# Optimization experiments

Measured on AMD Instinct MI355X. Metric: run time of the kernel, lower is better.

Reference implementation:

```python
import jax, jax.numpy as jnp
import numpy as np

B, S, H, NH = 2, 2048, 1024, 16
HD = H // NH  # head_dim = 64


def setup_inputs() -> dict:
    key = jax.random.key(0)
    k1, k2, k3 = jax.random.split(key, 3)
    x = jax.random.normal(k1, (B, S, H), dtype=jnp.float32)
    # additive causal mask: 0 on/below diagonal, -1e9 above
    causal = jnp.tril(jnp.ones((S, S), dtype=bool))
    mask = jnp.where(causal, 0.0, -1e9).astype(jnp.float32)[None, None, :, :]
    # fan-in scaled init like flax Dense default (lecun_normal)
    W_qkv = jax.random.normal(k2, (H, 3 * H), dtype=jnp.float32) / np.sqrt(H)
    W_out = jax.random.normal(k3, (H, H), dtype=jnp.float32) / np.sqrt(H)
    return {"x": x, "mask": mask, "W_qkv": W_qkv, "W_out": W_out}


def reference(x, mask, W_qkv, W_out):
    b, s, _ = x.shape
    qkv = jnp.einsum('bsh,hf->bsf', x, W_qkv)  # [B,S,3H]
    q, k, v = jnp.split(qkv, 3, axis=-1)
    q = q.reshape(b, s, NH, HD)
    k = k.reshape(b, s, NH, HD)
    v = v.reshape(b, s, NH, HD)
    scores = jnp.einsum('bqhd,bkhd->bhqk', q, k) / jnp.sqrt(jnp.float32(HD))
    scores = scores + mask
    attn = jax.nn.softmax(scores, axis=-1)
    y = jnp.einsum('bhqk,bkhd->bqhd', attn, v).reshape(b, s, H)
    return jnp.einsum('bsh,ho->bso', y, W_out)
```

## Files before the change

kernel.cpp:

```cpp
#include <hip/hip_runtime.h>

#define B_ 2
#define S_ 2048
#define H_ 1024
#define NH_ 16
#define HD_ 64

typedef short s16x8 __attribute__((ext_vector_type(8)));
typedef float f32x4 __attribute__((ext_vector_type(4)));

__device__ __forceinline__ ushort f2bf(float f) {
  union { float f; unsigned u; } v;
  v.f = f;
  unsigned r = (v.u + 0x7fffu + ((v.u >> 16) & 1u)) >> 16;
  return (ushort)r;
}

__device__ __forceinline__ void gload16(const void* g, void* l) {
  typedef const __attribute__((address_space(1))) unsigned int* gp_t;
  typedef __attribute__((address_space(3))) unsigned int* lp_t;
  __builtin_amdgcn_global_load_lds((gp_t)g, (lp_t)l, 16, 0, 0);
}

__global__ __launch_bounds__(256) void k_prep(const float* __restrict__ x,
                                              ushort* __restrict__ xb,
                                              const float* __restrict__ Wqkv,
                                              ushort* __restrict__ wqkvT,
                                              const float* __restrict__ Wout,
                                              ushort* __restrict__ woutT) {
  __shared__ ushort tile[32][33];
  const int bid = blockIdx.x;
  if (bid < 4096) {
    int i = bid * 256 + threadIdx.x;
    float4 v = ((const float4*)x)[i];
    ushort4 o;
    o.x = f2bf(v.x); o.y = f2bf(v.y); o.z = f2bf(v.z); o.w = f2bf(v.w);
    ((ushort4*)xb)[i] = o;
    return;
  }
  const float* in;
  ushort* out;
  int R = 1024, C, t;
  if (bid < 7168) { in = Wqkv; out = wqkvT; C = 3072; t = bid - 4096; }
  else            { in = Wout; out = woutT; C = 1024; t = bid - 7168; }
  int nbx = C >> 5;
  int c0 = (t % nbx) * 32, r0 = (t / nbx) * 32;
  int tr = threadIdx.x >> 5, tc = threadIdx.x & 31;
#pragma unroll
  for (int i = 0; i < 4; ++i)
    tile[tr + 8 * i][tc] = f2bf(in[(size_t)(r0 + tr + 8 * i) * C + c0 + tc]);
  __syncthreads();
#pragma unroll
  for (int i = 0; i < 4; ++i)
    out[(size_t)(c0 + tr + 8 * i) * R + r0 + tc] = tile[tc][tr + 8 * i];
}

template <int MODE>
__global__ __launch_bounds__(256) void k_gemm(const ushort* __restrict__ A,
                                              const ushort* __restrict__ Bt,
                                              void* __restrict__ out0,
                                              ushort* __restrict__ outK,
                                              ushort* __restrict__ outV,
                                              int Kdim, int Ndim) {
  __shared__ __align__(16) ushort As[2][128 * 64];
  __shared__ __align__(16) ushort Bs[2][128 * 64];
  const int nwg = gridDim.x * gridDim.y;
  const int id = blockIdx.y * gridDim.x + blockIdx.x;
  const int sid = (id & 7) * (nwg >> 3) + (id >> 3);
  const int m0 = (sid / gridDim.x) * 128, n0 = (sid % gridDim.x) * 128;
  const int tid = threadIdx.x, lane = tid & 63, w = tid >> 6;
  const int g = lane >> 4, c = lane & 15;
  const int wr = w >> 1, wc = w & 1;
  f32x4 acc[4][4] = {};
  const int trow = tid >> 3, tcol = tid & 7;
  const ushort* ag = A + (size_t)(m0 + trow) * Kdim + tcol * 8;
  const ushort* bg = Bt + (size_t)(n0 + trow) * Kdim + tcol * 8;

#define STAGE_G(bf, k0)                                      \
  do {                                                       \
    _Pragma("unroll") for (int i_ = 0; i_ < 4; ++i_) {       \
      gload16(ag + (k0) + i_ * 32 * Kdim, As[bf] + tid * 8 + i_ * 2048); \
      gload16(bg + (k0) + i_ * 32 * Kdim, Bs[bf] + tid * 8 + i_ * 2048); \
    }                                                        \
  } while (0)

  const int nk = Kdim >> 6;
  STAGE_G(0, 0);
  asm volatile("s_waitcnt vmcnt(0)" ::: "memory");
  __builtin_amdgcn_s_barrier();
  __builtin_amdgcn_sched_barrier(0);

  int buf = 0;
#pragma unroll 1
  for (int t = 0; t < nk; ++t) {
    if (t + 1 < nk) STAGE_G(buf ^ 1, (t + 1) * 64);
#pragma unroll
    for (int kk = 0; kk < 64; kk += 32) {
      s16x8 af[4], bfr[4];
#pragma unroll
      for (int i = 0; i < 4; ++i)
        af[i] = *(const s16x8*)(As[buf] + (wr * 64 + i * 16 + c) * 64 + kk + g * 8);
#pragma unroll
      for (int i = 0; i < 4; ++i)
        bfr[i] = *(const s16x8*)(Bs[buf] + (wc * 64 + i * 16 + c) * 64 + kk + g * 8);
      __builtin_amdgcn_s_setprio(1);
#pragma unroll
      for (int i = 0; i < 4; ++i)
#pragma unroll
        for (int j = 0; j < 4; ++j)
          acc[i][j] = __builtin_amdgcn_mfma_f32_16x16x32_bf16(af[i], bfr[j], acc[i][j], 0, 0, 0);
      __builtin_amdgcn_s_setprio(0);
    }
    asm volatile("s_waitcnt vmcnt(0)" ::: "memory");
    __builtin_amdgcn_s_barrier();
    __builtin_amdgcn_sched_barrier(0);
    buf ^= 1;
  }
#undef STAGE_G

  if (MODE == 1) {
    float* out = (float*)out0;
#pragma unroll
    for (int i = 0; i < 4; ++i) {
      int mb = m0 + wr * 64 + i * 16 + g * 4;
#pragma unroll
      for (int j = 0; j < 4; ++j) {
        int n = n0 + wc * 64 + j * 16 + c;
#pragma unroll
        for (int r = 0; r < 4; ++r)
          out[(size_t)(mb + r) * Ndim + n] = acc[i][j][r];
      }
    }
  } else {
    if (n0 < 1024) {
      const float ALPHA = 0.18033688f;
      ushort* outQ = (ushort*)out0;
#pragma unroll
      for (int i = 0; i < 4; ++i) {
        int mb = m0 + wr * 64 + i * 16 + g * 4;
#pragma unroll
        for (int j = 0; j < 4; ++j) {
          int n = n0 + wc * 64 + j * 16 + c;
#pragma unroll
          for (int r = 0; r < 4; ++r)
            outQ[(size_t)(mb + r) * 1024 + n] = f2bf(acc[i][j][r] * ALPHA);
        }
      }
    } else if (n0 < 2048) {
#pragma unroll
      for (int i = 0; i < 4; ++i) {
        int mb = m0 + wr * 64 + i * 16 + g * 4;
#pragma unroll
        for (int j = 0; j < 4; ++j) {
          int n = n0 - 1024 + wc * 64 + j * 16 + c;
#pragma unroll
          for (int r = 0; r < 4; ++r)
            outK[(size_t)(mb + r) * 1024 + n] = f2bf(acc[i][j][r]);
        }
      }
    } else {
#pragma unroll
      for (int i = 0; i < 4; ++i) {
        int mb = m0 + wr * 64 + i * 16 + g * 4;
        int bidx = mb >> 11;
        int s = mb & 2047;
#pragma unroll
        for (int j = 0; j < 4; ++j) {
          int nv = n0 - 2048 + wc * 64 + j * 16 + c;
          int h = nv >> 6, d = nv & 63;
          ushort4 pk;
          pk.x = f2bf(acc[i][j][0]);
          pk.y = f2bf(acc[i][j][1]);
          pk.z = f2bf(acc[i][j][2]);
          pk.w = f2bf(acc[i][j][3]);
          *(ushort4*)(outV + ((size_t)((bidx * 16 + h) * 64 + d)) * 2048 + s) = pk;
        }
      }
    }
  }
}

__global__ __launch_bounds__(256) void k_attn(const ushort* __restrict__ Qb,
                                              const ushort* __restrict__ Kb,
                                              const ushort* __restrict__ Vt,
                                              ushort* __restrict__ Yb) {
  __shared__ __align__(16) ushort Ks[2][64 * 64];
  __shared__ __align__(16) ushort Vs[2][64 * 64];
  __shared__ __align__(16) unsigned int Pp[4][16 * 32];
  const int fid = blockIdx.x;
  const int wid = (fid & 7) * 64 + (fid >> 3);
  const int bh = wid >> 4;
  const int j = wid & 15;
  const int b = bh >> 4, h = bh & 15;
  const int tid = threadIdx.x, w = tid >> 6, lane = tid & 63;
  const int g = lane >> 4, c = lane & 15;
  char* pb = (char*)(&Pp[w][0]);

  const int trow = tid >> 3, tcol = tid & 7;
  const int csrc = tcol ^ (trow & 7);
  const ushort* kgb = Kb + (size_t)(b * S_ + trow) * H_ + h * HD_ + csrc * 8;
  const ushort* vgb = Vt + (size_t)(bh * HD_ + trow) * S_ + csrc * 8;

#define STAGE(bf, tile)                                          \
  do {                                                           \
    int ks_ = (tile) * 64;                                       \
    gload16(kgb + (size_t)ks_ * H_, Ks[bf] + tid * 8);           \
    gload16(kgb + (size_t)(ks_ + 32) * H_, Ks[bf] + 2048 + tid * 8); \
    gload16(vgb + ks_, Vs[bf] + tid * 8);                        \
    gload16(vgb + ks_ + 32 * S_, Vs[bf] + 2048 + tid * 8);       \
  } while (0)

#pragma unroll 1
  for (int half = 0; half < 2; ++half) {
    const int qc = half ? (31 - j) : j;
    const int q0 = qc * 64;
    const int nt = qc + 1;
    const int qw = q0 + w * 16;

    s16x8 qf[2];
#pragma unroll
    for (int dc = 0; dc < 2; ++dc)
      qf[dc] = *(const s16x8*)(Qb + (size_t)(b * S_ + qw + c) * H_ +
                               h * HD_ + dc * 32 + g * 8);

    f32x4 oacc[4] = {};
    float m = -1e30f, lp = 0.f;

    STAGE(0, 0);
    asm volatile("s_waitcnt vmcnt(0)" ::: "memory");
    __builtin_amdgcn_s_barrier();
    __builtin_amdgcn_sched_barrier(0);

    int buf = 0;
#pragma unroll 1
    for (int it = 0; it < nt; ++it) {
      const int ks = it * 64;
      if (it + 1 < nt) STAGE(buf ^ 1, it + 1);

      f32x4 sacc[4] = {};
      __builtin_amdgcn_s_setprio(1);
#pragma unroll
      for (int dc = 0; dc < 2; ++dc) {
#pragma unroll
        for (int kt = 0; kt < 4; ++kt) {
          int R = kt * 16 + c;
          int cc = dc * 4 + g;
          s16x8 kf = *(const s16x8*)((const char*)Ks[buf] + R * 128 + ((cc ^ (R & 7)) << 4));
          sacc[kt] = __builtin_amdgcn_mfma_f32_16x16x32_bf16(kf, qf[dc], sacc[kt], 0, 0, 0);
        }
      }
      __builtin_amdgcn_s_setprio(0);

      if (it == nt - 1) {
        int q = qw + c;
#pragma unroll
        for (int kt = 0; kt < 4; ++kt)
#pragma unroll
          for (int r = 0; r < 4; ++r)
            if (ks + kt * 16 + g * 4 + r > q) sacc[kt][r] = -1e30f;
      }

      float t0 = fmaxf(fmaxf(sacc[0][0], sacc[0][1]), fmaxf(sacc[0][2], sacc[0][3]));
      float t1 = fmaxf(fmaxf(sacc[1][0], sacc[1][1]), fmaxf(sacc[1][2], sacc[1][3]));
      float t2 = fmaxf(fmaxf(sacc[2][0], sacc[2][1]), fmaxf(sacc[2][2], sacc[2][3]));
      float t3 = fmaxf(fmaxf(sacc[3][0], sacc[3][1]), fmaxf(sacc[3][2], sacc[3][3]));
      float t = fmaxf(fmaxf(t0, t1), fmaxf(t2, t3));
      t = fmaxf(t, __shfl_xor(t, 16));
      t = fmaxf(t, __shfl_xor(t, 32));

      if (__any(t > m + 8.0f)) {
        float mnew = fmaxf(m, t);
        float sc = __builtin_amdgcn_exp2f(m - mnew);
        m = mnew;
        lp *= sc;
        float scq[4];
#pragma unroll
        for (int r = 0; r < 4; ++r) scq[r] = __shfl(sc, g * 4 + r);
#pragma unroll
        for (int dt = 0; dt < 4; ++dt)
#pragma unroll
          for (int r = 0; r < 4; ++r) oacc[dt][r] *= scq[r];
      }

      float p[4][4];
      float rs = 0.f;
#pragma unroll
      for (int kt = 0; kt < 4; ++kt)
#pragma unroll
        for (int r = 0; r < 4; ++r) {
          p[kt][r] = __builtin_amdgcn_exp2f(sacc[kt][r] - m);
          rs += p[kt][r];
        }
      lp += rs;
      unsigned int pw[8];
#pragma unroll
      for (int kt = 0; kt < 4; ++kt) {
        asm("v_cvt_pk_bf16_f32 %0, %1, %2" : "=v"(pw[kt * 2 + 0]) : "v"(p[kt][0]), "v"(p[kt][1]));
        asm("v_cvt_pk_bf16_f32 %0, %1, %2" : "=v"(pw[kt * 2 + 1]) : "v"(p[kt][2]), "v"(p[kt][3]));
      }
#pragma unroll
      for (int kt = 0; kt < 4; ++kt) {
        int qd = kt * 2 + (g >> 1);
        *(uint2*)(pb + c * 128 + ((qd ^ (c & 7)) << 4) + ((g & 1) << 3)) =
            make_uint2(pw[kt * 2], pw[kt * 2 + 1]);
      }
      asm volatile("s_waitcnt lgkmcnt(0)" ::: "memory");
      __builtin_amdgcn_sched_barrier(0);

      __builtin_amdgcn_s_setprio(1);
#pragma unroll
      for (int kc = 0; kc < 2; ++kc) {
        int qd = kc * 4 + g;
        s16x8 pf = *(const s16x8*)(pb + c * 128 + ((qd ^ (c & 7)) << 4));
        int cc = kc * 4 + g;
#pragma unroll
        for (int dt = 0; dt < 4; ++dt) {
          int R = dt * 16 + c;
          s16x8 vf = *(const s16x8*)((const char*)Vs[buf] + R * 128 + ((cc ^ (R & 7)) << 4));
          oacc[dt] = __builtin_amdgcn_mfma_f32_16x16x32_bf16(pf, vf, oacc[dt], 0, 0, 0);
        }
      }
      __builtin_amdgcn_s_setprio(0);

      asm volatile("s_waitcnt vmcnt(0)" ::: "memory");
      __builtin_amdgcn_s_barrier();
      __builtin_amdgcn_sched_barrier(0);
      buf ^= 1;
    }

    float lt = lp;
    lt += __shfl_xor(lt, 16);
    lt += __shfl_xor(lt, 32);
    float rq[4];
#pragma unroll
    for (int r = 0; r < 4; ++r) rq[r] = 1.0f / __shfl(lt, g * 4 + r);
#pragma unroll
    for (int dt = 0; dt < 4; ++dt)
#pragma unroll
      for (int r = 0; r < 4; ++r) {
        int s = qw + g * 4 + r;
        Yb[(size_t)(b * S_ + s) * H_ + h * HD_ + dt * 16 + c] = f2bf(oacc[dt][r] * rq[r]);
      }
  }
#undef STAGE
}

extern "C" void kernel_launch(void* const* d_in, const int* in_sizes, int n_in,
                              void* d_out, int out_size, void* d_ws, size_t ws_size,
                              hipStream_t stream) {
  (void)in_sizes; (void)n_in; (void)out_size; (void)ws_size;
  const float* x = (const float*)d_in[0];
  const float* Wqkv = (const float*)d_in[2];
  const float* Wout = (const float*)d_in[3];
  float* out = (float*)d_out;

  char* ws = (char*)d_ws;
  ushort* xb    = (ushort*)(ws + 0);
  ushort* wqkvT = (ushort*)(ws + 8388608);
  ushort* woutT = (ushort*)(ws + 14680064);
  ushort* Qb    = (ushort*)(ws + 16777216);
  ushort* Kb    = (ushort*)(ws + 25165824);
  ushort* Vtb   = (ushort*)(ws + 33554432);
  ushort* Yb    = (ushort*)(ws + 41943040);

  k_prep<<<dim3(8192), dim3(256), 0, stream>>>(x, xb, Wqkv, wqkvT, Wout, woutT);
  k_gemm<0><<<dim3(24, 32), dim3(256), 0, stream>>>(xb, wqkvT, (void*)Qb, Kb, Vtb, 1024, 3072);
  k_attn<<<dim3(512), dim3(256), 0, stream>>>(Qb, Kb, Vtb, Yb);
  k_gemm<1><<<dim3(8, 32), dim3(256), 0, stream>>>(Yb, woutT, (void*)out, nullptr, nullptr, 1024, 1024);
}
```

Measured before the change: 209.5 us.

## Enlarge GEMM tiles to 256x256 with swizzled LDS and interleaved prefetch

Rewrites both projection GEMMs to use 256x256 output tiles with 512-thread blocks and 8 waves. Shared memory uses an XOR-swizzled layout to avoid bank conflicts. Next-tile global-to-LDS loads are split into four stripes and issued between quadrant compute phases, with finer waitcnt and barrier control. This raises reuse of each loaded tile and overlaps loads with MFMA work. The cost is far fewer blocks: 192 for the QKV GEMM and only 64 for the output GEMM, which may leave many CUs idle.

```diff
diff --git a/kernel.cpp b/kernel.cpp
--- a/kernel.cpp
+++ b/kernel.cpp
@@ -56,76 +56,107 @@
 }
 
 template <int MODE>
-__global__ __launch_bounds__(256) void k_gemm(const ushort* __restrict__ A,
-                                              const ushort* __restrict__ Bt,
-                                              void* __restrict__ out0,
-                                              ushort* __restrict__ outK,
-                                              ushort* __restrict__ outV,
-                                              int Kdim, int Ndim) {
-  __shared__ __align__(16) ushort As[2][128 * 64];
-  __shared__ __align__(16) ushort Bs[2][128 * 64];
+__global__ __launch_bounds__(512, 2) void k_gemm(const ushort* __restrict__ A,
+                                                 const ushort* __restrict__ Bt,
+                                                 void* __restrict__ out0,
+                                                 ushort* __restrict__ outK,
+                                                 ushort* __restrict__ outV,
+                                                 int Kdim, int Ndim) {
+  __shared__ __align__(16) ushort As[2][256 * 64];
+  __shared__ __align__(16) ushort Bs[2][256 * 64];
   const int nwg = gridDim.x * gridDim.y;
   const int id = blockIdx.y * gridDim.x + blockIdx.x;
   const int sid = (id & 7) * (nwg >> 3) + (id >> 3);
-  const int m0 = (sid / gridDim.x) * 128, n0 = (sid % gridDim.x) * 128;
+  const int m0 = (sid / gridDim.x) * 256, n0 = (sid % gridDim.x) * 256;
   const int tid = threadIdx.x, lane = tid & 63, w = tid >> 6;
   const int g = lane >> 4, c = lane & 15;
-  const int wr = w >> 1, wc = w & 1;
-  f32x4 acc[4][4] = {};
-  const int trow = tid >> 3, tcol = tid & 7;
-  const ushort* ag = A + (size_t)(m0 + trow) * Kdim + tcol * 8;
-  const ushort* bg = Bt + (size_t)(n0 + trow) * Kdim + tcol * 8;
-
-#define STAGE_G(bf, k0)                                      \
-  do {                                                       \
-    _Pragma("unroll") for (int i_ = 0; i_ < 4; ++i_) {       \
-      gload16(ag + (k0) + i_ * 32 * Kdim, As[bf] + tid * 8 + i_ * 2048); \
-      gload16(bg + (k0) + i_ * 32 * Kdim, Bs[bf] + tid * 8 + i_ * 2048); \
-    }                                                        \
-  } while (0)
-
-  const int nk = Kdim >> 6;
-  STAGE_G(0, 0);
-  asm volatile("s_waitcnt vmcnt(0)" ::: "memory");
+  const int wm = w >> 2, wn = w & 3;
+  f32x4 acc[8][4] = {};
+
+  const int srow = tid >> 3;
+  const int csrc = (tid & 7) ^ (srow & 7);
+  const ushort* ag = A + (size_t)(m0 + srow) * Kdim + csrc * 8;
+  const ushort* bg = Bt + (size_t)(n0 + srow) * Kdim + csrc * 8;
+  const int nT = Kdim >> 6;
+
+#define STRIPE(gp, ro, T_, dst) \
+  gload16((gp) + (size_t)(ro) * Kdim + (T_) * 64, (dst) + tid * 8)
+
+  STRIPE(ag, 0, 0, As[0]); STRIPE(ag, 64, 0, As[0] + 4096);
+  STRIPE(bg, 0, 0, Bs[0]); STRIPE(bg, 64, 0, Bs[0] + 4096);
+  STRIPE(bg, 128, 0, Bs[0] + 8192); STRIPE(bg, 192, 0, Bs[0] + 12288);
+  STRIPE(ag, 128, 0, As[0] + 8192); STRIPE(ag, 192, 0, As[0] + 12288);
+  asm volatile("s_waitcnt vmcnt(4)" ::: "memory");
   __builtin_amdgcn_s_barrier();
   __builtin_amdgcn_sched_barrier(0);
 
-  int buf = 0;
 #pragma unroll 1
-  for (int t = 0; t < nk; ++t) {
-    if (t + 1 < nk) STAGE_G(buf ^ 1, (t + 1) * 64);
-#pragma unroll
-    for (int kk = 0; kk < 64; kk += 32) {
-      s16x8 af[4], bfr[4];
-#pragma unroll
-      for (int i = 0; i < 4; ++i)
-        af[i] = *(const s16x8*)(As[buf] + (wr * 64 + i * 16 + c) * 64 + kk + g * 8);
-#pragma unroll
-      for (int i = 0; i < 4; ++i)
-        bfr[i] = *(const s16x8*)(Bs[buf] + (wc * 64 + i * 16 + c) * 64 + kk + g * 8);
+  for (int t = 0; t < nT; ++t) {
+    const char* Ab = (const char*)As[t & 1];
+    const char* Bb = (const char*)Bs[t & 1];
+    const bool stg = (t + 1 < nT);
+    const int T2 = t + 1, bf2 = T2 & 1;
+#pragma unroll
+    for (int q = 0; q < 4; ++q) {
+      const int ih = q >> 1, jh = q & 1;
+      s16x8 af[4][2], bfr[2][2];
+#pragma unroll
+      for (int i2 = 0; i2 < 4; ++i2) {
+        int row = ih * 128 + wm * 64 + i2 * 16 + c;
+#pragma unroll
+        for (int kk = 0; kk < 2; ++kk) {
+          int ch = g + kk * 4;
+          af[i2][kk] = *(const s16x8*)(Ab + row * 128 + ((ch ^ (row & 7)) << 4));
+        }
+      }
+#pragma unroll
+      for (int j2 = 0; j2 < 2; ++j2) {
+        int row = jh * 128 + wn * 32 + j2 * 16 + c;
+#pragma unroll
+        for (int kk = 0; kk < 2; ++kk) {
+          int ch = g + kk * 4;
+          bfr[j2][kk] = *(const s16x8*)(Bb + row * 128 + ((ch ^ (row & 7)) << 4));
+        }
+      }
+      if (stg) {
+        if (q == 0) { STRIPE(ag, 0, T2, As[bf2]);          STRIPE(ag, 64, T2, As[bf2] + 4096); }
+        if (q == 1) { STRIPE(bg, 0, T2, Bs[bf2]);          STRIPE(bg, 64, T2, Bs[bf2] + 4096); }
+        if (q == 2) { STRIPE(bg, 128, T2, Bs[bf2] + 8192); STRIPE(bg, 192, T2, Bs[bf2] + 12288); }
+        if (q == 3) { STRIPE(ag, 128, T2, As[bf2] + 8192); STRIPE(ag, 192, T2, As[bf2] + 12288); }
+      }
+      __builtin_amdgcn_s_barrier();
+      asm volatile("s_waitcnt lgkmcnt(0)" ::: "memory");
+      __builtin_amdgcn_sched_barrier(0);
       __builtin_amdgcn_s_setprio(1);
 #pragma unroll
-      for (int i = 0; i < 4; ++i)
-#pragma unroll
-        for (int j = 0; j < 4; ++j)
-          acc[i][j] = __builtin_amdgcn_mfma_f32_16x16x32_bf16(af[i], bfr[j], acc[i][j], 0, 0, 0);
+      for (int i2 = 0; i2 < 4; ++i2)
+#pragma unroll
+        for (int j2 = 0; j2 < 2; ++j2)
+#pragma unroll
+          for (int kk = 0; kk < 2; ++kk)
+            acc[ih * 4 + i2][jh * 2 + j2] = __builtin_amdgcn_mfma_f32_16x16x32_bf16(
+                af[i2][kk], bfr[j2][kk], acc[ih * 4 + i2][jh * 2 + j2], 0, 0, 0);
       __builtin_amdgcn_s_setprio(0);
+      if (stg) {
+        if (q != 2) asm volatile("s_waitcnt vmcnt(4)" ::: "memory");
+      } else {
+        if (q == 0) asm volatile("s_waitcnt vmcnt(2)" ::: "memory");
+        else if (q == 1) asm volatile("s_waitcnt vmcnt(0)" ::: "memory");
+      }
+      __builtin_amdgcn_s_barrier();
+      __builtin_amdgcn_sched_barrier(0);
     }
-    asm volatile("s_waitcnt vmcnt(0)" ::: "memory");
-    __builtin_amdgcn_s_barrier();
-    __builtin_amdgcn_sched_barrier(0);
-    buf ^= 1;
   }
-#undef STAGE_G
+#undef STRIPE
 
   if (MODE == 1) {
     float* out = (float*)out0;
 #pragma unroll
-    for (int i = 0; i < 4; ++i) {
-      int mb = m0 + wr * 64 + i * 16 + g * 4;
+    for (int i = 0; i < 8; ++i) {
+      int mb = m0 + (i >> 2) * 128 + wm * 64 + (i & 3) * 16 + g * 4;
 #pragma unroll
       for (int j = 0; j < 4; ++j) {
-        int n = n0 + wc * 64 + j * 16 + c;
+        int n = n0 + (j >> 1) * 128 + wn * 32 + (j & 1) * 16 + c;
 #pragma unroll
         for (int r = 0; r < 4; ++r)
           out[(size_t)(mb + r) * Ndim + n] = acc[i][j][r];
@@ -136,11 +167,11 @@
       const float ALPHA = 0.18033688f;
       ushort* outQ = (ushort*)out0;
 #pragma unroll
-      for (int i = 0; i < 4; ++i) {
-        int mb = m0 + wr * 64 + i * 16 + g * 4;
+      for (int i = 0; i < 8; ++i) {
+        int mb = m0 + (i >> 2) * 128 + wm * 64 + (i & 3) * 16 + g * 4;
 #pragma unroll
         for (int j = 0; j < 4; ++j) {
-          int n = n0 + wc * 64 + j * 16 + c;
+          int n = n0 + (j >> 1) * 128 + wn * 32 + (j & 1) * 16 + c;
 #pragma unroll
           for (int r = 0; r < 4; ++r)
             outQ[(size_t)(mb + r) * 1024 + n] = f2bf(acc[i][j][r] * ALPHA);
@@ -148,11 +179,11 @@
       }
     } else if (n0 < 2048) {
 #pragma unroll
-      for (int i = 0; i < 4; ++i) {
-        int mb = m0 + wr * 64 + i * 16 + g * 4;
+      for (int i = 0; i < 8; ++i) {
+        int mb = m0 + (i >> 2) * 128 + wm * 64 + (i & 3) * 16 + g * 4;
 #pragma unroll
         for (int j = 0; j < 4; ++j) {
-          int n = n0 - 1024 + wc * 64 + j * 16 + c;
+          int n = n0 - 1024 + (j >> 1) * 128 + wn * 32 + (j & 1) * 16 + c;
 #pragma unroll
           for (int r = 0; r < 4; ++r)
             outK[(size_t)(mb + r) * 1024 + n] = f2bf(acc[i][j][r]);
@@ -160,13 +191,13 @@
       }
     } else {
 #pragma unroll
-      for (int i = 0; i < 4; ++i) {
-        int mb = m0 + wr * 64 + i * 16 + g * 4;
+      for (int i = 0; i < 8; ++i) {
+        int mb = m0 + (i >> 2) * 128 + wm * 64 + (i & 3) * 16 + g * 4;
         int bidx = mb >> 11;
         int s = mb & 2047;
 #pragma unroll
         for (int j = 0; j < 4; ++j) {
-          int nv = n0 - 2048 + wc * 64 + j * 16 + c;
+          int nv = n0 - 2048 + (j >> 1) * 128 + wn * 32 + (j & 1) * 16 + c;
           int h = nv >> 6, d = nv & 63;
           ushort4 pk;
           pk.x = f2bf(acc[i][j][0]);
@@ -364,7 +395,7 @@
   ushort* Yb    = (ushort*)(ws + 41943040);
 
   k_prep<<<dim3(8192), dim3(256), 0, stream>>>(x, xb, Wqkv, wqkvT, Wout, woutT);
-  k_gemm<0><<<dim3(24, 32), dim3(256), 0, stream>>>(xb, wqkvT, (void*)Qb, Kb, Vtb, 1024, 3072);
+  k_gemm<0><<<dim3(12, 16), dim3(512), 0, stream>>>(xb, wqkvT, (void*)Qb, Kb, Vtb, 1024, 3072);
   k_attn<<<dim3(512), dim3(256), 0, stream>>>(Qb, Kb, Vtb, Yb);
-  k_gemm<1><<<dim3(8, 32), dim3(256), 0, stream>>>(Yb, woutT, (void*)out, nullptr, nullptr, 1024, 1024);
-}
+  k_gemm<1><<<dim3(4, 16), dim3(512), 0, stream>>>(Yb, woutT, (void*)out, nullptr, nullptr, 1024, 1024);
+}
```

After: 214.2 us. +2.2%, slower.
